# Performance work log

Hardware: AMD Instinct MI355X
Metric: run time of the kernel (lower is better)

## Reference

```python
import jax, jax.numpy as jnp
import numpy as np

B, S, E, C = 128, 512, 768, 9


def setup_inputs() -> dict:
    key = jax.random.key(0)
    ks = jax.random.split(key, 7)
    return {
        "enc": jax.random.normal(ks[0], (B, S, E), dtype=jnp.float32),
        "W": jax.random.normal(ks[1], (C, E), dtype=jnp.float32) * 0.02,
        "b": jax.random.normal(ks[2], (C,), dtype=jnp.float32) * 0.02,
        "start_transitions": jax.random.normal(ks[3], (C,), dtype=jnp.float32) * 0.1,
        "end_transitions": jax.random.normal(ks[4], (C,), dtype=jnp.float32) * 0.1,
        "transitions": jax.random.normal(ks[5], (C, C), dtype=jnp.float32) * 0.1,
        "tags": jax.random.randint(ks[6], (B, S), 0, C, dtype=jnp.int64),
        "mask": jnp.ones((B, S), dtype=bool),
    }


def _crf_nll_mean(emissions, tags, mask, start_transitions, end_transitions, transitions):
    # emissions: [B,S,C], tags: [B,S] int, mask: [B,S] bool (mask[:,0] all True)
    maskf = mask.astype(emissions.dtype)
    b_idx = jnp.arange(emissions.shape[0])
    # ---- numerator: score of the gold tag path ----
    em_tag = jnp.take_along_axis(emissions, tags[..., None], axis=2)[..., 0]  # [B,S]
    trans_pair = transitions[tags[:, :-1], tags[:, 1:]]  # [B,S-1]
    num = start_transitions[tags[:, 0]] + em_tag[:, 0]
    num = num + jnp.sum((trans_pair + em_tag[:, 1:]) * maskf[:, 1:], axis=1)
    seq_len = mask.sum(axis=1).astype(jnp.int32)
    last_tags = tags[b_idx, seq_len - 1]
    num = num + end_transitions[last_tags]
    # ---- denominator: forward algorithm (log partition) via scan ----
    def step(alpha, xs):
        em_t, m_t = xs  # [B,C], [B]
        # broadcast: alpha[b,i] + transitions[i,j] + em_t[b,j]
        nxt = jax.nn.logsumexp(alpha[:, :, None] + transitions[None, :, :] + em_t[:, None, :], axis=1)
        alpha = jnp.where(m_t[:, None], nxt, alpha)
        return alpha, None

    alpha0 = start_transitions[None, :] + emissions[:, 0]  # [B,C]
    em_rest = jnp.swapaxes(emissions[:, 1:], 0, 1)  # [S-1,B,C]
    m_rest = jnp.swapaxes(mask[:, 1:], 0, 1)        # [S-1,B]
    alpha, _ = jax.lax.scan(step, alpha0, (em_rest, m_rest))
    den = jax.nn.logsumexp(alpha + end_transitions[None, :], axis=1)  # [B]
    # reduction='mean' over batch; module returns -llh
    return jnp.mean(den - num)


def reference(enc, W, b, start_transitions, end_transitions, transitions, tags, mask):
    # BERT output `enc` is frozen (torch.no_grad); dropout omitted (deterministic ref)
    emissions = jnp.einsum("bse,ce->bsc", enc, W) + b  # linear head [B,S,C]
    return _crf_nll_mean(emissions, tags, mask, start_transitions, end_transitions, transitions)
```

## Files before the change

### kernel.cpp

```cpp
#include <hip/hip_runtime.h>

static constexpr int kB = 128;
static constexpr int kS = 512;
static constexpr int kE = 768;
static constexpr int kC = 9;
static constexpr int kRows = kB * kS;
static constexpr int kT = 16;
static constexpr int kChunks = 32;

__global__ __launch_bounds__(256) void emis_kernel(const float* __restrict__ enc,
                                                   const float* __restrict__ W,
                                                   const float* __restrict__ bias,
                                                   float* __restrict__ em) {
  const int lane = threadIdx.x & 63;
  const int wave = (blockIdx.x * blockDim.x + threadIdx.x) >> 6;
  const int nwaves = (gridDim.x * blockDim.x) >> 6;

  float w[kC][12];
#pragma unroll
  for (int c = 0; c < kC; ++c) {
#pragma unroll
    for (int ch = 0; ch < 3; ++ch) {
      const float4 f = *reinterpret_cast<const float4*>(W + c * kE + ch * 256 + lane * 4);
      w[c][ch * 4 + 0] = f.x; w[c][ch * 4 + 1] = f.y;
      w[c][ch * 4 + 2] = f.z; w[c][ch * 4 + 3] = f.w;
    }
  }
  const float bc = (lane < kC) ? bias[lane] : 0.f;

  for (int row = wave; row < kRows; row += nwaves) {
    const float* rp = enc + (size_t)row * kE;
    float x[12];
#pragma unroll
    for (int ch = 0; ch < 3; ++ch) {
      const float4 f = *reinterpret_cast<const float4*>(rp + ch * 256 + lane * 4);
      x[ch * 4 + 0] = f.x; x[ch * 4 + 1] = f.y;
      x[ch * 4 + 2] = f.z; x[ch * 4 + 3] = f.w;
    }
    float acc[kC];
#pragma unroll
    for (int c = 0; c < kC; ++c) {
      float a = 0.f;
#pragma unroll
      for (int k = 0; k < 12; ++k) a = fmaf(x[k], w[c][k], a);
      acc[c] = a;
    }
#pragma unroll
    for (int m = 1; m < 64; m <<= 1) {
#pragma unroll
      for (int c = 0; c < kC; ++c) acc[c] += __shfl_xor(acc[c], m, 64);
    }
    if (lane < kC) {
      float v = acc[0];
#pragma unroll
      for (int c = 1; c < kC; ++c) v = (lane == c) ? acc[c] : v;
      em[(size_t)row * kC + lane] = v + bc;
    }
  }
}

__global__ __launch_bounds__(256) void num_kernel(const float* __restrict__ em,
                                                  const int* __restrict__ tags,
                                                  const float* __restrict__ trans,
                                                  const float* __restrict__ start_t,
                                                  const float* __restrict__ end_t,
                                                  float* __restrict__ num_out) {
  const int b = blockIdx.x;
  const int tid = threadIdx.x;
  const int* tg = tags + b * kS;
  const float* eb = em + (size_t)b * kS * kC;

  float local = 0.f;
  for (int t = tid; t < kS; t += 256) {
    const int ct = tg[t];
    const float e = eb[t * kC + ct];
    if (t == 0) local += start_t[ct] + e;
    else        local += trans[tg[t - 1] * kC + ct] + e;
  }
#pragma unroll
  for (int m = 32; m >= 1; m >>= 1) local += __shfl_down(local, m, 64);
  __shared__ float sm[4];
  if ((tid & 63) == 0) sm[tid >> 6] = local;
  __syncthreads();
  if (tid == 0) {
    num_out[b] = sm[0] + sm[1] + sm[2] + sm[3] + end_t[tg[kS - 1]];
  }
}

__global__ __launch_bounds__(128) void chunk_kernel(const float* __restrict__ em,
                                                    const float* __restrict__ trans,
                                                    float* __restrict__ Pout) {
  const int blk = blockIdx.x;
  const int b = blk >> 5;
  const int k = blk & 31;
  const int tid = threadIdx.x;
  const bool act = tid < 81;
  const int i = act ? (tid / 9) : 0;
  const int j = act ? (tid % 9) : 0;

  __shared__ float P[81];

  const float* eb = em + (size_t)b * kS * kC;
  const int t0 = 1 + k * kT;
  const int t1 = min(kS, t0 + kT);

  float tr[kC];
  if (act) {
#pragma unroll
    for (int kk = 0; kk < kC; ++kk) tr[kk] = trans[kk * kC + j];
    P[tid] = trans[i * kC + j] + eb[t0 * kC + j];
  }
  __syncthreads();

  for (int t = t0 + 1; t < t1; ++t) {
    float nv = 0.f;
    if (act) {
      const float em_t = eb[t * kC + j];
      float v[kC];
      float m = -3.0e38f;
#pragma unroll
      for (int kk = 0; kk < kC; ++kk) {
        v[kk] = P[i * kC + kk] + tr[kk];
        m = fmaxf(m, v[kk]);
      }
      float s = 0.f;
#pragma unroll
      for (int kk = 0; kk < kC; ++kk) s += __expf(v[kk] - m);
      nv = m + __logf(s) + em_t;
    }
    __syncthreads();
    if (act) P[tid] = nv;
    __syncthreads();
  }

  if (act) Pout[(size_t)blk * 81 + j * kC + i] = P[tid];
}

__global__ __launch_bounds__(64) void combine_kernel(const float* __restrict__ Pmat,
                                                     const float* __restrict__ em,
                                                     const float* __restrict__ start_t,
                                                     const float* __restrict__ end_t,
                                                     float* __restrict__ den_out) {
  const int b = blockIdx.x;
  const int lane = threadIdx.x;
  if (lane >= kC) return;

  float alpha = start_t[lane] + em[(size_t)b * kS * kC + lane];
  const float* Pb = Pmat + (size_t)b * kChunks * 81;

  for (int k = 0; k < kChunks; ++k) {
    const float* P = Pb + k * 81 + lane * kC;
    float p[kC];
#pragma unroll
    for (int i = 0; i < kC; ++i) p[i] = P[i];
    float tv[kC];
    float m = -3.0e38f;
#pragma unroll
    for (int i = 0; i < kC; ++i) {
      const float ai = __shfl(alpha, i, 64);
      tv[i] = ai + p[i];
      m = fmaxf(m, tv[i]);
    }
    float s = 0.f;
#pragma unroll
    for (int i = 0; i < kC; ++i) s += __expf(tv[i] - m);
    alpha = m + __logf(s);
  }

  const float v = alpha + end_t[lane];
  float vv[kC];
  float m = -3.0e38f;
#pragma unroll
  for (int i = 0; i < kC; ++i) {
    vv[i] = __shfl(v, i, 64);
    m = fmaxf(m, vv[i]);
  }
  float s = 0.f;
#pragma unroll
  for (int i = 0; i < kC; ++i) s += __expf(vv[i] - m);
  if (lane == 0) den_out[b] = m + __logf(s);
}

__global__ __launch_bounds__(128) void final_kernel(const float* __restrict__ den,
                                                    const float* __restrict__ num,
                                                    float* __restrict__ out) {
  const int tid = threadIdx.x;
  float v = den[tid] - num[tid];
#pragma unroll
  for (int m = 32; m >= 1; m >>= 1) v += __shfl_down(v, m, 64);
  __shared__ float sm[2];
  if ((tid & 63) == 0) sm[tid >> 6] = v;
  __syncthreads();
  if (tid == 0) out[0] = (sm[0] + sm[1]) * (1.0f / (float)kB);
}

extern "C" void kernel_launch(void* const* d_in, const int* in_sizes, int n_in,
                              void* d_out, int out_size, void* d_ws, size_t ws_size,
                              hipStream_t stream) {
  const float* enc   = (const float*)d_in[0];
  const float* W     = (const float*)d_in[1];
  const float* bias  = (const float*)d_in[2];
  const float* start = (const float*)d_in[3];
  const float* end_t = (const float*)d_in[4];
  const float* trans = (const float*)d_in[5];
  const int*   tags  = (const int*)d_in[6];

  float* em   = (float*)d_ws;
  float* Pmat = em + (size_t)kRows * kC;
  float* den  = Pmat + (size_t)kB * kChunks * 81;
  float* num  = den + kB;
  float* out  = (float*)d_out;

  hipLaunchKernelGGL(emis_kernel, dim3(2048), dim3(256), 0, stream, enc, W, bias, em);
  hipLaunchKernelGGL(num_kernel, dim3(kB), dim3(256), 0, stream, em, tags, trans, start, end_t, num);
  hipLaunchKernelGGL(chunk_kernel, dim3(kB * kChunks), dim3(128), 0, stream, em, trans, Pmat);
  hipLaunchKernelGGL(combine_kernel, dim3(kB), dim3(64), 0, stream, Pmat, em, start, end_t, den);
  hipLaunchKernelGGL(final_kernel, dim3(1), dim3(128), 0, stream, den, num, out);
}
```

Before: 328.6 us.

## Fuse bf16 MFMA emission projection and numerator into per-chunk CRF kernel

```diff
diff --git a/kernel.cpp b/kernel.cpp
--- a/kernel.cpp
+++ b/kernel.cpp
@@ -4,155 +4,149 @@
 static constexpr int kS = 512;
 static constexpr int kE = 768;
 static constexpr int kC = 9;
-static constexpr int kRows = kB * kS;
 static constexpr int kT = 16;
 static constexpr int kChunks = 32;
-
-__global__ __launch_bounds__(256) void emis_kernel(const float* __restrict__ enc,
-                                                   const float* __restrict__ W,
-                                                   const float* __restrict__ bias,
-                                                   float* __restrict__ em) {
-  const int lane = threadIdx.x & 63;
-  const int wave = (blockIdx.x * blockDim.x + threadIdx.x) >> 6;
-  const int nwaves = (gridDim.x * blockDim.x) >> 6;
-
-  float w[kC][12];
-#pragma unroll
-  for (int c = 0; c < kC; ++c) {
-#pragma unroll
-    for (int ch = 0; ch < 3; ++ch) {
-      const float4 f = *reinterpret_cast<const float4*>(W + c * kE + ch * 256 + lane * 4);
-      w[c][ch * 4 + 0] = f.x; w[c][ch * 4 + 1] = f.y;
-      w[c][ch * 4 + 2] = f.z; w[c][ch * 4 + 3] = f.w;
-    }
-  }
-  const float bc = (lane < kC) ? bias[lane] : 0.f;
-
-  for (int row = wave; row < kRows; row += nwaves) {
-    const float* rp = enc + (size_t)row * kE;
-    float x[12];
-#pragma unroll
-    for (int ch = 0; ch < 3; ++ch) {
-      const float4 f = *reinterpret_cast<const float4*>(rp + ch * 256 + lane * 4);
-      x[ch * 4 + 0] = f.x; x[ch * 4 + 1] = f.y;
-      x[ch * 4 + 2] = f.z; x[ch * 4 + 3] = f.w;
-    }
-    float acc[kC];
-#pragma unroll
-    for (int c = 0; c < kC; ++c) {
-      float a = 0.f;
-#pragma unroll
-      for (int k = 0; k < 12; ++k) a = fmaf(x[k], w[c][k], a);
-      acc[c] = a;
-    }
-#pragma unroll
-    for (int m = 1; m < 64; m <<= 1) {
-#pragma unroll
-      for (int c = 0; c < kC; ++c) acc[c] += __shfl_xor(acc[c], m, 64);
-    }
-    if (lane < kC) {
-      float v = acc[0];
-#pragma unroll
-      for (int c = 1; c < kC; ++c) v = (lane == c) ? acc[c] : v;
-      em[(size_t)row * kC + lane] = v + bc;
-    }
-  }
-}
-
-__global__ __launch_bounds__(256) void num_kernel(const float* __restrict__ em,
-                                                  const int* __restrict__ tags,
-                                                  const float* __restrict__ trans,
-                                                  const float* __restrict__ start_t,
-                                                  const float* __restrict__ end_t,
-                                                  float* __restrict__ num_out) {
-  const int b = blockIdx.x;
-  const int tid = threadIdx.x;
-  const int* tg = tags + b * kS;
-  const float* eb = em + (size_t)b * kS * kC;
-
-  float local = 0.f;
-  for (int t = tid; t < kS; t += 256) {
-    const int ct = tg[t];
-    const float e = eb[t * kC + ct];
-    if (t == 0) local += start_t[ct] + e;
-    else        local += trans[tg[t - 1] * kC + ct] + e;
-  }
-#pragma unroll
-  for (int m = 32; m >= 1; m >>= 1) local += __shfl_down(local, m, 64);
-  __shared__ float sm[4];
-  if ((tid & 63) == 0) sm[tid >> 6] = local;
-  __syncthreads();
-  if (tid == 0) {
-    num_out[b] = sm[0] + sm[1] + sm[2] + sm[3] + end_t[tg[kS - 1]];
-  }
-}
-
-__global__ __launch_bounds__(128) void chunk_kernel(const float* __restrict__ em,
-                                                    const float* __restrict__ trans,
-                                                    float* __restrict__ Pout) {
+static constexpr int kWpad = kE + 8;
+
+using bf16x8 = __attribute__((ext_vector_type(8))) short;
+using f32x4  = __attribute__((ext_vector_type(4))) float;
+
+__device__ __forceinline__ unsigned short f2bf(float f) {
+  union { float f; unsigned u; } cv; cv.f = f;
+  return (unsigned short)((cv.u + 0x7FFFu + ((cv.u >> 16) & 1u)) >> 16);
+}
+
+__global__ __launch_bounds__(128) void fused_chunk(
+    const float* __restrict__ enc, const float* __restrict__ W,
+    const float* __restrict__ bias, const float* __restrict__ trans,
+    const float* __restrict__ start_t, const float* __restrict__ end_t,
+    const int* __restrict__ tags, float* __restrict__ Pout,
+    float* __restrict__ numP) {
+  __shared__ unsigned short Wl[16 * kWpad];
+  __shared__ float emt[kT * 12];
+  __shared__ float P[81];
+  __shared__ float atmp[16];
+  __shared__ float nred[kT];
+
   const int blk = blockIdx.x;
   const int b = blk >> 5;
   const int k = blk & 31;
   const int tid = threadIdx.x;
+
+  for (int idx = tid; idx < kC * kE; idx += 128) {
+    const int c = idx / kE, e = idx - c * kE;
+    Wl[c * kWpad + e] = f2bf(W[idx]);
+  }
+  __syncthreads();
+
+  if (tid < 64) {
+    const int mn = tid & 15;
+    const int quad = tid >> 4;
+    const float* rp = enc + ((size_t)(b * kS + k * kT + mn)) * kE + quad * 8;
+    const unsigned short* wp = Wl + mn * kWpad + quad * 8;
+    f32x4 acc = {0.f, 0.f, 0.f, 0.f};
+#pragma unroll
+    for (int s = 0; s < kE / 32; ++s) {
+      const float4 x0 = *reinterpret_cast<const float4*>(rp + s * 32);
+      const float4 x1 = *reinterpret_cast<const float4*>(rp + s * 32 + 4);
+      bf16x8 a;
+      a[0] = (short)f2bf(x0.x); a[1] = (short)f2bf(x0.y);
+      a[2] = (short)f2bf(x0.z); a[3] = (short)f2bf(x0.w);
+      a[4] = (short)f2bf(x1.x); a[5] = (short)f2bf(x1.y);
+      a[6] = (short)f2bf(x1.z); a[7] = (short)f2bf(x1.w);
+      const bf16x8 bf = *reinterpret_cast<const bf16x8*>(wp + s * 32);
+      acc = __builtin_amdgcn_mfma_f32_16x16x32_bf16(a, bf, acc, 0, 0, 0);
+    }
+    if (mn < kC) {
+      const float bc = bias[mn];
+#pragma unroll
+      for (int r = 0; r < 4; ++r) emt[(quad * 4 + r) * 12 + mn] = acc[r] + bc;
+    }
+  }
+  __syncthreads();
+
+  if (tid < kT) {
+    const int t = k * kT + tid;
+    const int ct = tags[b * kS + t];
+    float v = emt[tid * 12 + ct];
+    if (t == 0) v += start_t[ct];
+    else        v += trans[tags[b * kS + t - 1] * kC + ct];
+    if (t == kS - 1) v += end_t[ct];
+    nred[tid] = v;
+  }
+  __syncthreads();
+  if (tid == 0) {
+    float s = 0.f;
+#pragma unroll
+    for (int i = 0; i < kT; ++i) s += nred[i];
+    numP[blk] = s;
+  }
+
   const bool act = tid < 81;
-  const int i = act ? (tid / 9) : 0;
-  const int j = act ? (tid % 9) : 0;
-
-  __shared__ float P[81];
-
-  const float* eb = em + (size_t)b * kS * kC;
-  const int t0 = 1 + k * kT;
-  const int t1 = min(kS, t0 + kT);
-
+  const int ci = act ? (tid / 9) : 0;
+  const int cj = act ? (tid - ci * 9) : 0;
   float tr[kC];
   if (act) {
 #pragma unroll
-    for (int kk = 0; kk < kC; ++kk) tr[kk] = trans[kk * kC + j];
-    P[tid] = trans[i * kC + j] + eb[t0 * kC + j];
-  }
-  __syncthreads();
-
-  for (int t = t0 + 1; t < t1; ++t) {
-    float nv = 0.f;
-    if (act) {
-      const float em_t = eb[t * kC + j];
-      float v[kC];
-      float m = -3.0e38f;
-#pragma unroll
-      for (int kk = 0; kk < kC; ++kk) {
-        v[kk] = P[i * kC + kk] + tr[kk];
-        m = fmaxf(m, v[kk]);
+    for (int kk = 0; kk < kC; ++kk) tr[kk] = trans[kk * kC + cj];
+  }
+
+  if (k == 0) {
+    if (tid < kC) atmp[tid] = start_t[tid] + emt[tid];
+    __syncthreads();
+    for (int t = 1; t < kT; ++t) {
+      float nv = 0.f;
+      if (tid < kC) {
+        float m = -3.0e38f, v[kC];
+#pragma unroll
+        for (int i = 0; i < kC; ++i) { v[i] = atmp[i] + tr[i]; m = fmaxf(m, v[i]); }
+        float s = 0.f;
+#pragma unroll
+        for (int i = 0; i < kC; ++i) s += __expf(v[i] - m);
+        nv = m + __logf(s) + emt[t * 12 + tid];
       }
-      float s = 0.f;
-#pragma unroll
-      for (int kk = 0; kk < kC; ++kk) s += __expf(v[kk] - m);
-      nv = m + __logf(s) + em_t;
-    }
+      __syncthreads();
+      if (tid < kC) atmp[tid] = nv;
+      __syncthreads();
+    }
+    if (tid < kC) Pout[(size_t)blk * 81 + tid] = atmp[tid];
+  } else {
+    if (act) P[tid] = trans[ci * kC + cj] + emt[cj];
     __syncthreads();
-    if (act) P[tid] = nv;
-    __syncthreads();
-  }
-
-  if (act) Pout[(size_t)blk * 81 + j * kC + i] = P[tid];
+    for (int t = 1; t < kT; ++t) {
+      float nv = 0.f;
+      if (act) {
+        float m = -3.0e38f, v[kC];
+#pragma unroll
+        for (int kk = 0; kk < kC; ++kk) { v[kk] = P[ci * 9 + kk] + tr[kk]; m = fmaxf(m, v[kk]); }
+        float s = 0.f;
+#pragma unroll
+        for (int kk = 0; kk < kC; ++kk) s += __expf(v[kk] - m);
+        nv = m + __logf(s) + emt[t * 12 + cj];
+      }
+      __syncthreads();
+      if (act) P[tid] = nv;
+      __syncthreads();
+    }
+    if (act) Pout[(size_t)blk * 81 + cj * kC + ci] = P[tid];
+  }
 }
 
 __global__ __launch_bounds__(64) void combine_kernel(const float* __restrict__ Pmat,
-                                                     const float* __restrict__ em,
-                                                     const float* __restrict__ start_t,
                                                      const float* __restrict__ end_t,
                                                      float* __restrict__ den_out) {
   const int b = blockIdx.x;
   const int lane = threadIdx.x;
   if (lane >= kC) return;
 
-  float alpha = start_t[lane] + em[(size_t)b * kS * kC + lane];
   const float* Pb = Pmat + (size_t)b * kChunks * 81;
-
-  for (int k = 0; k < kChunks; ++k) {
-    const float* P = Pb + k * 81 + lane * kC;
+  float alpha = Pb[lane];
+
+  for (int k = 1; k < kChunks; ++k) {
+    const float* Pk = Pb + k * 81 + lane * kC;
     float p[kC];
 #pragma unroll
-    for (int i = 0; i < kC; ++i) p[i] = P[i];
+    for (int i = 0; i < kC; ++i) p[i] = Pk[i];
     float tv[kC];
     float m = -3.0e38f;
 #pragma unroll
@@ -182,10 +176,13 @@
 }
 
 __global__ __launch_bounds__(128) void final_kernel(const float* __restrict__ den,
-                                                    const float* __restrict__ num,
+                                                    const float* __restrict__ numP,
                                                     float* __restrict__ out) {
   const int tid = threadIdx.x;
-  float v = den[tid] - num[tid];
+  float s = 0.f;
+#pragma unroll
+  for (int k = 0; k < kChunks; ++k) s += numP[tid * kChunks + k];
+  float v = den[tid] - s;
 #pragma unroll
   for (int m = 32; m >= 1; m >>= 1) v += __shfl_down(v, m, 64);
   __shared__ float sm[2];
@@ -205,15 +202,13 @@
   const float* trans = (const float*)d_in[5];
   const int*   tags  = (const int*)d_in[6];
 
-  float* em   = (float*)d_ws;
-  float* Pmat = em + (size_t)kRows * kC;
-  float* den  = Pmat + (size_t)kB * kChunks * 81;
-  float* num  = den + kB;
+  float* Pmat = (float*)d_ws;
+  float* numP = Pmat + (size_t)kB * kChunks * 81;
+  float* den  = numP + kB * kChunks;
   float* out  = (float*)d_out;
 
-  hipLaunchKernelGGL(emis_kernel, dim3(2048), dim3(256), 0, stream, enc, W, bias, em);
-  hipLaunchKernelGGL(num_kernel, dim3(kB), dim3(256), 0, stream, em, tags, trans, start, end_t, num);
-  hipLaunchKernelGGL(chunk_kernel, dim3(kB * kChunks), dim3(128), 0, stream, em, trans, Pmat);
-  hipLaunchKernelGGL(combine_kernel, dim3(kB), dim3(64), 0, stream, Pmat, em, start, end_t, den);
-  hipLaunchKernelGGL(final_kernel, dim3(1), dim3(128), 0, stream, den, num, out);
-}
+  hipLaunchKernelGGL(fused_chunk, dim3(kB * kChunks), dim3(128), 0, stream,
+                     enc, W, bias, trans, start, end_t, tags, Pmat, numP);
+  hipLaunchKernelGGL(combine_kernel, dim3(kB), dim3(64), 0, stream, Pmat, end_t, den);
+  hipLaunchKernelGGL(final_kernel, dim3(1), dim3(128), 0, stream, den, numP, out);
+}
```

Result: no change. 327.7 us (-0.3%).
